# Performance work log

Hardware: AMD Instinct MI355X
Metric: run time of the kernel (lower is better)

Reference implementation:

```python
import jax, jax.numpy as jnp
import numpy as np

B, S, D = 8, 2048, 1024


def setup_inputs() -> dict:
    key = jax.random.key(0)
    k1, k2, k3, k4, k5 = jax.random.split(key, 5)
    scale = 1.0 / np.sqrt(D)
    x = jax.random.normal(k1, (B, S, D), dtype=jnp.float32)
    Wq = jax.random.normal(k2, (D, D), dtype=jnp.float32) * scale
    Wk = jax.random.normal(k3, (D, D), dtype=jnp.float32) * scale
    Wv = jax.random.normal(k4, (D, D), dtype=jnp.float32) * scale
    # sequence lengths in [1, S]
    lens = jax.random.randint(k5, (B,), 1, S + 1, dtype=jnp.int32)
    return {"x": x, "lens": lens, "Wq": Wq, "Wk": Wk, "Wv": Wv}


def reference(x, lens, Wq, Wk, Wv):
    # nn.Linear(bias=False): y = x @ W.T
    q = jnp.einsum('bsd,ed->bse', x, Wq)
    k = jnp.einsum('bsd,ed->bse', x, Wk)
    v = jnp.einsum('bsd,ed->bse', x, Wv)
    # scores: QK^T / sqrt(D)  -> [B, S, S]
    scores = jnp.einsum('bqd,bkd->bqk', q, k) / jnp.sqrt(jnp.asarray(D, x.dtype))
    # key-padding mask from lens: True where key position >= len (masked to -inf)
    key_pad = jnp.arange(S)[None, :] >= lens[:, None]          # [B, S]
    scores = jnp.where(key_pad[:, None, :], -jnp.inf, scores)  # broadcast over query dim
    att = jax.nn.softmax(scores, axis=2)
    return jnp.einsum('bqk,bkd->bqd', att, v)
```

## Files before the change

### kernel.cpp

```cpp
#include <hip/hip_runtime.h>
#include <stdint.h>

typedef __bf16 bf16;
typedef __bf16 bf16x8 __attribute__((ext_vector_type(8)));
typedef __bf16 bf16x4 __attribute__((ext_vector_type(4)));
typedef float f32x4 __attribute__((ext_vector_type(4)));
typedef float f32x16 __attribute__((ext_vector_type(16)));

#define DEV static __device__ __forceinline__

DEV void async_copy16(const bf16* gsrc, const bf16* ldst) {
  __builtin_amdgcn_global_load_lds(
      (__attribute__((address_space(1))) void*)(uintptr_t)gsrc,
      (__attribute__((address_space(3))) void*)(uint32_t)(uintptr_t)ldst,
      16, 0, 0);
}

DEV void gemm_tile16(const bf16* __restrict__ A, const bf16* __restrict__ B,
                     int lda, int ldb, int kTiles,
                     bf16* As, bf16* Bs, f32x4 acc[4][4]) {
  const int tid  = threadIdx.x;
  const int wave = tid >> 6;
  const int lane = tid & 63;
  const int wm = (wave >> 1) * 64;
  const int wn = (wave & 1) * 64;
  const int mf = lane & 15;
  const int jb = lane >> 4;
  const int sw = (mf & 7) * 8;

  const int srow = tid >> 3;
  const int scol = ((tid & 7) ^ (srow & 7)) * 8;
  const bf16* Ag = A + (size_t)srow * lda + scol;
  const bf16* Bg = B + (size_t)srow * ldb + scol;
  bf16* Asw = As + wave * 512;
  bf16* Bsw = Bs + wave * 512;

  for (int kt = 0; kt < kTiles; ++kt) {
    __syncthreads();
    const bf16* ag = Ag + kt * 64;
    const bf16* bg = Bg + kt * 64;
#pragma unroll
    for (int i = 0; i < 4; ++i) {
      async_copy16(ag + (size_t)(i * 32) * lda, Asw + i * 2048);
      async_copy16(bg + (size_t)(i * 32) * ldb, Bsw + i * 2048);
    }
    __syncthreads();
#pragma unroll
    for (int ks = 0; ks < 2; ++ks) {
      const int j8 = (ks * 4 + jb) * 8;
      bf16x8 af[4], bv[4];
#pragma unroll
      for (int i = 0; i < 4; ++i)
        af[i] = *(const bf16x8*)&As[(wm + i * 16 + mf) * 64 + (j8 ^ sw)];
#pragma unroll
      for (int j = 0; j < 4; ++j)
        bv[j] = *(const bf16x8*)&Bs[(wn + j * 16 + mf) * 64 + (j8 ^ sw)];
#pragma unroll
      for (int i = 0; i < 4; ++i)
#pragma unroll
        for (int j = 0; j < 4; ++j)
          acc[i][j] = __builtin_amdgcn_mfma_f32_16x16x32_bf16(af[i], bv[j], acc[i][j], 0, 0, 0);
    }
  }
}

DEV void gemm_tile32(const bf16* __restrict__ A, const bf16* __restrict__ B,
                     int lda, int ldb, int kTiles,
                     bf16* As, bf16* Bs, f32x16 acc[2][2]) {
  const int tid  = threadIdx.x;
  const int wave = tid >> 6;
  const int lane = tid & 63;
  const int wm = (wave >> 1) * 64;
  const int wn = (wave & 1) * 64;
  const int rf = lane & 31;
  const int kh = (lane >> 5) * 8;
  const int sw = (lane & 7) * 8;

  const int srow = tid >> 3;
  const int scol = ((tid & 7) ^ (srow & 7)) * 8;
  const bf16* Ag = A + (size_t)srow * lda + scol;
  const bf16* Bg = B + (size_t)srow * ldb + scol;
  bf16* Asw = As + wave * 512;
  bf16* Bsw = Bs + wave * 512;

  for (int kt = 0; kt < kTiles; ++kt) {
    __syncthreads();
    const bf16* ag = Ag + kt * 64;
    const bf16* bg = Bg + kt * 64;
#pragma unroll
    for (int i = 0; i < 4; ++i) {
      async_copy16(ag + (size_t)(i * 32) * lda, Asw + i * 2048);
      async_copy16(bg + (size_t)(i * 32) * ldb, Bsw + i * 2048);
    }
    __syncthreads();
#pragma unroll
    for (int ks = 0; ks < 4; ++ks) {
      const int off = (ks * 16 + kh) ^ sw;
      bf16x8 a0 = *(const bf16x8*)&As[(wm + rf) * 64 + off];
      bf16x8 a1 = *(const bf16x8*)&As[(wm + 32 + rf) * 64 + off];
      bf16x8 b0 = *(const bf16x8*)&Bs[(wn + rf) * 64 + off];
      bf16x8 b1 = *(const bf16x8*)&Bs[(wn + 32 + rf) * 64 + off];
      acc[0][0] = __builtin_amdgcn_mfma_f32_32x32x16_bf16(a0, b0, acc[0][0], 0, 0, 0);
      acc[0][1] = __builtin_amdgcn_mfma_f32_32x32x16_bf16(a0, b1, acc[0][1], 0, 0, 0);
      acc[1][0] = __builtin_amdgcn_mfma_f32_32x32x16_bf16(a1, b0, acc[1][0], 0, 0, 0);
      acc[1][1] = __builtin_amdgcn_mfma_f32_32x32x16_bf16(a1, b1, acc[1][1], 0, 0, 0);
    }
  }
}

#define EPILOGUE16(STMT)                                                     \
  do {                                                                       \
    const int lane = threadIdx.x & 63, wave = threadIdx.x >> 6;              \
    const int colb = n0 + (wave & 1) * 64 + (lane & 15);                     \
    const int rowb = m0 + (wave >> 1) * 64 + (lane >> 4) * 4;                \
    _Pragma("unroll") for (int i = 0; i < 4; ++i)                            \
      _Pragma("unroll") for (int r = 0; r < 4; ++r) {                        \
        size_t row = rowb + i * 16 + r;                                      \
        _Pragma("unroll") for (int j = 0; j < 4; ++j) {                      \
          size_t col = colb + j * 16;                                        \
          float val = acc[i][j][r];                                          \
          STMT;                                                              \
        }                                                                    \
      }                                                                      \
  } while (0)

#define EPILOGUE32(STMT)                                                     \
  do {                                                                       \
    const int lane = threadIdx.x & 63, wave = threadIdx.x >> 6;              \
    const int colb = n0 + (wave & 1) * 64 + (lane & 31);                     \
    const int rowb = m0 + (wave >> 1) * 64 + (lane >> 5) * 4;                \
    _Pragma("unroll") for (int i = 0; i < 2; ++i)                            \
      _Pragma("unroll") for (int reg = 0; reg < 16; ++reg) {                 \
        size_t row = rowb + i * 32 + (reg & 3) + 8 * (reg >> 2);             \
        _Pragma("unroll") for (int j = 0; j < 2; ++j) {                      \
          size_t col = colb + j * 32;                                        \
          float val = acc[i][j][reg];                                        \
          STMT;                                                              \
        }                                                                    \
      }                                                                      \
  } while (0)

__global__ __launch_bounds__(256) void k_cast_all(const float* __restrict__ X,
                                                  const float* __restrict__ Wq,
                                                  const float* __restrict__ Wk,
                                                  const float* __restrict__ Wv,
                                                  bf16* __restrict__ Xb,
                                                  bf16* __restrict__ Wb) {
  int i = blockIdx.x * 256 + threadIdx.x;
  const float* src;
  bf16* dst;
  int off;
  if (i < 4194304) {
    src = X; dst = Xb; off = i;
  } else {
    int j = i - 4194304;
    int which = j >> 18;
    src = (which == 0) ? Wq : ((which == 1) ? Wk : Wv);
    dst = Wb + (size_t)(j >> 18) * 1048576;
    off = j & 262143;
  }
  float4 v = ((const float4*)src)[off];
  bf16x4 o = {(bf16)v.x, (bf16)v.y, (bf16)v.z, (bf16)v.w};
  ((bf16x4*)dst)[off] = o;
}

__global__ __launch_bounds__(256) void k_gemm_qkv(const bf16* __restrict__ X,
                                                  const bf16* __restrict__ W,
                                                  const int* __restrict__ lens,
                                                  bf16* __restrict__ QKV) {
  const int n0 = blockIdx.x * 128;
  const int m0 = blockIdx.y * 128;
  if (n0 >= 1024 && (m0 & 2047) >= lens[m0 >> 11]) return;
  __shared__ __align__(16) bf16 As[128 * 64];
  __shared__ __align__(16) bf16 Bs[128 * 64];
  f32x4 acc[4][4] = {};
  gemm_tile16(X + (size_t)m0 * 1024, W + (size_t)n0 * 1024, 1024, 1024, 16, As, Bs, acc);
  const float qscale = (n0 < 1024) ? 0.03125f : 1.0f;
  EPILOGUE16(QKV[row * 3072 + col] = (bf16)(val * qscale));
}

__global__ __launch_bounds__(256) void k_transpose_v(const bf16* __restrict__ QKV,
                                                     const int* __restrict__ lens,
                                                     bf16* __restrict__ Vt) {
  __shared__ bf16 tile[32][33];
  const int b = blockIdx.z;
  const int s0 = blockIdx.x * 32;
  if (s0 >= ((lens[b] + 63) & ~63)) return;
  const int d0 = blockIdx.y * 32;
  const int tx = threadIdx.x, ty = threadIdx.y;
#pragma unroll
  for (int i = 0; i < 4; ++i)
    tile[ty + i * 8][tx] = QKV[(size_t)(b * 2048 + s0 + ty + i * 8) * 3072 + 2048 + d0 + tx];
  __syncthreads();
#pragma unroll
  for (int i = 0; i < 4; ++i)
    Vt[(size_t)(b * 1024 + d0 + ty + i * 8) * 2048 + s0 + tx] = tile[tx][ty + i * 8];
}

__global__ __launch_bounds__(256) void k_gemm_scores(const bf16* __restrict__ QKV,
                                                     const int* __restrict__ lens,
                                                     bf16* __restrict__ S) {
  const int b = blockIdx.z;
  const int len = lens[b];
  const int n0 = blockIdx.x * 128;
  if (n0 >= len) return;
  const int m0 = blockIdx.y * 128;
  __shared__ __align__(16) bf16 As[128 * 64];
  __shared__ __align__(16) bf16 Bs[128 * 64];
  const bf16* Q = QKV + (size_t)b * 2048 * 3072;
  const bf16* K = Q + 1024;
  f32x16 acc[2][2] = {};
  gemm_tile32(Q + (size_t)m0 * 3072, K + (size_t)n0 * 3072, 3072, 3072, 16, As, Bs, acc);
  bf16* Sb = S + (size_t)b * 2048 * 2048;
  EPILOGUE32(Sb[row * 2048 + col] = (bf16)val);
}

__global__ __launch_bounds__(256) void k_softmax(bf16* __restrict__ S,
                                                 const int* __restrict__ lens) {
  const int row = blockIdx.x;
  const int len = lens[row >> 11];
  const int kmax = (len + 63) & ~63;
  bf16* Sr = S + (size_t)row * 2048;
  const int tid = threadIdx.x;
  const int base = tid * 8;
  __shared__ float red[4];

  float f[8];
  if (base < len) {
    bf16x8 v = ((const bf16x8*)Sr)[tid];
#pragma unroll
    for (int e = 0; e < 8; ++e) f[e] = (base + e < len) ? (float)v[e] : -1e30f;
  } else {
#pragma unroll
    for (int e = 0; e < 8; ++e) f[e] = -1e30f;
  }
  float m = -1e30f;
#pragma unroll
  for (int e = 0; e < 8; ++e) m = fmaxf(m, f[e]);
#pragma unroll
  for (int off = 32; off; off >>= 1) m = fmaxf(m, __shfl_xor(m, off));
  if ((tid & 63) == 0) red[tid >> 6] = m;
  __syncthreads();
  m = fmaxf(fmaxf(red[0], red[1]), fmaxf(red[2], red[3]));
  __syncthreads();

  float s = 0.f;
#pragma unroll
  for (int e = 0; e < 8; ++e) {
    float p = (base + e < len) ? __expf(f[e] - m) : 0.f;
    f[e] = p;
    s += p;
  }
#pragma unroll
  for (int off = 32; off; off >>= 1) s += __shfl_xor(s, off);
  if ((tid & 63) == 0) red[tid >> 6] = s;
  __syncthreads();
  s = red[0] + red[1] + red[2] + red[3];
  const float inv = 1.f / s;

  if (base < kmax) {
    bf16x8 o;
#pragma unroll
    for (int e = 0; e < 8; ++e) o[e] = (bf16)(f[e] * inv);
    ((bf16x8*)Sr)[tid] = o;
  }
}

__global__ __launch_bounds__(256) void k_gemm_out(const bf16* __restrict__ P,
                                                  const bf16* __restrict__ Vt,
                                                  const int* __restrict__ lens,
                                                  float* __restrict__ Out) {
  const int b = blockIdx.z;
  const int kTiles = (lens[b] + 63) >> 6;
  const int n0 = blockIdx.x * 128;
  const int m0 = blockIdx.y * 128;
  __shared__ __align__(16) bf16 As[128 * 64];
  __shared__ __align__(16) bf16 Bs[128 * 64];
  const bf16* Pb = P + (size_t)b * 2048 * 2048;
  const bf16* Vb = Vt + (size_t)b * 1024 * 2048;
  f32x16 acc[2][2] = {};
  gemm_tile32(Pb + (size_t)m0 * 2048, Vb + (size_t)n0 * 2048, 2048, 2048, kTiles, As, Bs, acc);
  float* Ob = Out + (size_t)b * 2048 * 1024;
  EPILOGUE32(Ob[row * 1024 + col] = val);
}

extern "C" void kernel_launch(void* const* d_in, const int* in_sizes, int n_in,
                              void* d_out, int out_size, void* d_ws, size_t ws_size,
                              hipStream_t stream) {
  const float* x   = (const float*)d_in[0];
  const int* lens  = (const int*)d_in[1];
  const float* Wq  = (const float*)d_in[2];
  const float* Wk  = (const float*)d_in[3];
  const float* Wv  = (const float*)d_in[4];
  float* out = (float*)d_out;

  char* ws = (char*)d_ws;
  bf16* S   = (bf16*)(ws);
  bf16* Xb  = (bf16*)(ws);
  bf16* Wb  = (bf16*)(ws + 33554432);
  bf16* QKV = (bf16*)(ws + 67108864);
  bf16* Vt  = (bf16*)(ws + 167772160);

  k_cast_all<<<19456, 256, 0, stream>>>(x, Wq, Wk, Wv, Xb, Wb);
  k_gemm_qkv<<<dim3(24, 128), 256, 0, stream>>>(Xb, Wb, lens, QKV);
  k_transpose_v<<<dim3(64, 32, 8), dim3(32, 8), 0, stream>>>(QKV, lens, Vt);
  k_gemm_scores<<<dim3(16, 16, 8), 256, 0, stream>>>(QKV, lens, S);
  k_softmax<<<16384, 256, 0, stream>>>(S, lens);
  k_gemm_out<<<dim3(8, 16, 8), 256, 0, stream>>>(S, Vt, lens, out);
}
```

Baseline: 359.6 us.

## Rewrite QKV GEMM with 256x256 tiles, double-buffered async LDS loads

The QKV projection GEMM moves from 128x128 tiles with 256 threads and a single LDS buffer to 256x256 tiles with 512 threads and a K-step of 32. Global-to-LDS async copies are double-buffered, so the load for step t+2 is issued while step t computes, with explicit waitcnt and barriers. MFMA issue runs at raised wave priority. The larger tiles raise operand reuse per load, at the cost of higher register use (32 accumulators per wave), coarser padding skip, and fewer blocks for the machine to spread across CUs.

```diff
diff --git a/kernel.cpp b/kernel.cpp
--- a/kernel.cpp
+++ b/kernel.cpp
@@ -14,54 +14,6 @@
       (__attribute__((address_space(1))) void*)(uintptr_t)gsrc,
       (__attribute__((address_space(3))) void*)(uint32_t)(uintptr_t)ldst,
       16, 0, 0);
-}
-
-DEV void gemm_tile16(const bf16* __restrict__ A, const bf16* __restrict__ B,
-                     int lda, int ldb, int kTiles,
-                     bf16* As, bf16* Bs, f32x4 acc[4][4]) {
-  const int tid  = threadIdx.x;
-  const int wave = tid >> 6;
-  const int lane = tid & 63;
-  const int wm = (wave >> 1) * 64;
-  const int wn = (wave & 1) * 64;
-  const int mf = lane & 15;
-  const int jb = lane >> 4;
-  const int sw = (mf & 7) * 8;
-
-  const int srow = tid >> 3;
-  const int scol = ((tid & 7) ^ (srow & 7)) * 8;
-  const bf16* Ag = A + (size_t)srow * lda + scol;
-  const bf16* Bg = B + (size_t)srow * ldb + scol;
-  bf16* Asw = As + wave * 512;
-  bf16* Bsw = Bs + wave * 512;
-
-  for (int kt = 0; kt < kTiles; ++kt) {
-    __syncthreads();
-    const bf16* ag = Ag + kt * 64;
-    const bf16* bg = Bg + kt * 64;
-#pragma unroll
-    for (int i = 0; i < 4; ++i) {
-      async_copy16(ag + (size_t)(i * 32) * lda, Asw + i * 2048);
-      async_copy16(bg + (size_t)(i * 32) * ldb, Bsw + i * 2048);
-    }
-    __syncthreads();
-#pragma unroll
-    for (int ks = 0; ks < 2; ++ks) {
-      const int j8 = (ks * 4 + jb) * 8;
-      bf16x8 af[4], bv[4];
-#pragma unroll
-      for (int i = 0; i < 4; ++i)
-        af[i] = *(const bf16x8*)&As[(wm + i * 16 + mf) * 64 + (j8 ^ sw)];
-#pragma unroll
-      for (int j = 0; j < 4; ++j)
-        bv[j] = *(const bf16x8*)&Bs[(wn + j * 16 + mf) * 64 + (j8 ^ sw)];
-#pragma unroll
-      for (int i = 0; i < 4; ++i)
-#pragma unroll
-        for (int j = 0; j < 4; ++j)
-          acc[i][j] = __builtin_amdgcn_mfma_f32_16x16x32_bf16(af[i], bv[j], acc[i][j], 0, 0, 0);
-    }
-  }
 }
 
 DEV void gemm_tile32(const bf16* __restrict__ A, const bf16* __restrict__ B,
@@ -107,22 +59,6 @@
     }
   }
 }
-
-#define EPILOGUE16(STMT)                                                     \
-  do {                                                                       \
-    const int lane = threadIdx.x & 63, wave = threadIdx.x >> 6;              \
-    const int colb = n0 + (wave & 1) * 64 + (lane & 15);                     \
-    const int rowb = m0 + (wave >> 1) * 64 + (lane >> 4) * 4;                \
-    _Pragma("unroll") for (int i = 0; i < 4; ++i)                            \
-      _Pragma("unroll") for (int r = 0; r < 4; ++r) {                        \
-        size_t row = rowb + i * 16 + r;                                      \
-        _Pragma("unroll") for (int j = 0; j < 4; ++j) {                      \
-          size_t col = colb + j * 16;                                        \
-          float val = acc[i][j][r];                                          \
-          STMT;                                                              \
-        }                                                                    \
-      }                                                                      \
-  } while (0)
 
 #define EPILOGUE32(STMT)                                                     \
   do {                                                                       \
@@ -164,19 +100,93 @@
   ((bf16x4*)dst)[off] = o;
 }
 
-__global__ __launch_bounds__(256) void k_gemm_qkv(const bf16* __restrict__ X,
-                                                  const bf16* __restrict__ W,
-                                                  const int* __restrict__ lens,
-                                                  bf16* __restrict__ QKV) {
-  const int n0 = blockIdx.x * 128;
-  const int m0 = blockIdx.y * 128;
+__global__ __launch_bounds__(512, 2) void k_gemm_qkv(
+    const bf16* __restrict__ X, const bf16* __restrict__ W,
+    const int* __restrict__ lens, bf16* __restrict__ QKV) {
+  const int n0 = blockIdx.x * 256;
+  const int m0 = blockIdx.y * 256;
   if (n0 >= 1024 && (m0 & 2047) >= lens[m0 >> 11]) return;
-  __shared__ __align__(16) bf16 As[128 * 64];
-  __shared__ __align__(16) bf16 Bs[128 * 64];
-  f32x4 acc[4][4] = {};
-  gemm_tile16(X + (size_t)m0 * 1024, W + (size_t)n0 * 1024, 1024, 1024, 16, As, Bs, acc);
+  __shared__ __align__(16) char smem[65536];
+
+  const int tid = threadIdx.x;
+  const int lane = tid & 63, wid = tid >> 6;
+
+  int grow0, gcol0, grow1, gcol1;
+  {
+    int g = tid, rho = g >> 3, sig = (g & 7) ^ (rho & 7);
+    grow0 = 2 * rho + (sig >> 2); gcol0 = (sig & 3) * 8;
+    g = tid + 512; rho = g >> 3; sig = (g & 7) ^ (rho & 7);
+    grow1 = 2 * rho + (sig >> 2); gcol1 = (sig & 3) * 8;
+  }
+  const bf16* pa0 = X + (size_t)(m0 + grow0) * 1024 + gcol0;
+  const bf16* pa1 = X + (size_t)(m0 + grow1) * 1024 + gcol1;
+  const bf16* pb0 = W + (size_t)(n0 + grow0) * 1024 + gcol0;
+  const bf16* pb1 = W + (size_t)(n0 + grow1) * 1024 + gcol1;
+
+#define QKV_STAGE(kt, slot)                                  \
+  do {                                                       \
+    const int ko_ = (kt) * 32;                               \
+    char* sb_ = smem + (slot) * 32768 + wid * 1024;          \
+    async_copy16(pa0 + ko_, (const bf16*)sb_);               \
+    async_copy16(pa1 + ko_, (const bf16*)(sb_ + 8192));      \
+    async_copy16(pb0 + ko_, (const bf16*)(sb_ + 16384));     \
+    async_copy16(pb1 + ko_, (const bf16*)(sb_ + 24576));     \
+  } while (0)
+
+  const int mf = lane & 15, jb = lane >> 4;
+  const int wm = (wid >> 2) * 128, wn = (wid & 3) * 64;
+  const uint32_t pbyte = (uint32_t)((((((mf & 1) << 2) | jb) ^ ((mf >> 1) & 7))) * 16);
+  const uint32_t laneA = (uint32_t)(wm * 64 + (mf >> 1) * 128) + pbyte;
+  const uint32_t laneB = 16384u + (uint32_t)(wn * 64 + (mf >> 1) * 128) + pbyte;
+
+  f32x4 acc[8][4] = {};
+
+  QKV_STAGE(0, 0);
+  QKV_STAGE(1, 1);
+  asm volatile("s_waitcnt vmcnt(4)" ::: "memory");
+  __builtin_amdgcn_sched_barrier(0);
+  __builtin_amdgcn_s_barrier();
+  __builtin_amdgcn_sched_barrier(0);
+
+  for (int t = 0; t < 32; ++t) {
+    const char* As = smem + (t & 1) * 32768 + laneA;
+    const char* Bs = smem + (t & 1) * 32768 + laneB;
+    bf16x8 af[8], bfr[4];
+#pragma unroll
+    for (int i = 0; i < 8; ++i) af[i] = *(const bf16x8*)(As + i * 1024);
+#pragma unroll
+    for (int j = 0; j < 4; ++j) bfr[j] = *(const bf16x8*)(Bs + j * 1024);
+    __builtin_amdgcn_s_setprio(1);
+#pragma unroll
+    for (int i = 0; i < 8; ++i)
+#pragma unroll
+      for (int j = 0; j < 4; ++j)
+        acc[i][j] = __builtin_amdgcn_mfma_f32_16x16x32_bf16(af[i], bfr[j], acc[i][j], 0, 0, 0);
+    __builtin_amdgcn_s_setprio(0);
+    asm volatile("s_waitcnt lgkmcnt(0)" ::: "memory");
+    __builtin_amdgcn_sched_barrier(0);
+    __builtin_amdgcn_s_barrier();
+    __builtin_amdgcn_sched_barrier(0);
+    const int nx = (t + 2 < 32) ? t + 2 : 31;
+    QKV_STAGE(nx, t & 1);
+    asm volatile("s_waitcnt vmcnt(4)" ::: "memory");
+    __builtin_amdgcn_sched_barrier(0);
+    __builtin_amdgcn_s_barrier();
+    __builtin_amdgcn_sched_barrier(0);
+  }
+#undef QKV_STAGE
+
   const float qscale = (n0 < 1024) ? 0.03125f : 1.0f;
-  EPILOGUE16(QKV[row * 3072 + col] = (bf16)(val * qscale));
+  const int colb = n0 + wn + mf;
+  const int rowb = m0 + wm + jb * 4;
+#pragma unroll
+  for (int i = 0; i < 8; ++i)
+#pragma unroll
+    for (int r = 0; r < 4; ++r) {
+      bf16* dst = QKV + (size_t)(rowb + i * 16 + r) * 3072 + colb;
+#pragma unroll
+      for (int j = 0; j < 4; ++j) dst[j * 16] = (bf16)(acc[i][j][r] * qscale);
+    }
 }
 
 __global__ __launch_bounds__(256) void k_transpose_v(const bf16* __restrict__ QKV,
@@ -302,7 +312,7 @@
   bf16* Vt  = (bf16*)(ws + 167772160);
 
   k_cast_all<<<19456, 256, 0, stream>>>(x, Wq, Wk, Wv, Xb, Wb);
-  k_gemm_qkv<<<dim3(24, 128), 256, 0, stream>>>(Xb, Wb, lens, QKV);
+  k_gemm_qkv<<<dim3(12, 64), 512, 0, stream>>>(Xb, Wb, lens, QKV);
   k_transpose_v<<<dim3(64, 32, 8), dim3(32, 8), 0, stream>>>(QKV, lens, Vt);
   k_gemm_scores<<<dim3(16, 16, 8), 256, 0, stream>>>(QKV, lens, S);
   k_softmax<<<16384, 256, 0, stream>>>(S, lens);
```

New measurement: 385.9 us. +7.3%, slower.

## Compute V transposed directly via Wv·Xᵀ GEMM, drop transpose kernel

Applied to the files above, without the earlier changes.

V is no longer produced by the QKV projection and then transposed. A separate GEMM computes Vt = Wv · Xbᵀ per batch and writes it directly in the transposed layout that the output GEMM consumes. This removes the transpose kernel and the round trip of V through global memory, and it narrows the QK buffer to a 2048-column stride. In exchange it adds one kernel launch and changes how padding rows are skipped: V tiles are now culled by the rounded-up length in the N dimension rather than by the row length.

```diff
diff --git a/kernel.cpp b/kernel.cpp
--- a/kernel.cpp
+++ b/kernel.cpp
@@ -167,7 +167,7 @@
 __global__ __launch_bounds__(256) void k_gemm_qkv(const bf16* __restrict__ X,
                                                   const bf16* __restrict__ W,
                                                   const int* __restrict__ lens,
-                                                  bf16* __restrict__ QKV) {
+                                                  bf16* __restrict__ QK) {
   const int n0 = blockIdx.x * 128;
   const int m0 = blockIdx.y * 128;
   if (n0 >= 1024 && (m0 & 2047) >= lens[m0 >> 11]) return;
@@ -176,28 +176,27 @@
   f32x4 acc[4][4] = {};
   gemm_tile16(X + (size_t)m0 * 1024, W + (size_t)n0 * 1024, 1024, 1024, 16, As, Bs, acc);
   const float qscale = (n0 < 1024) ? 0.03125f : 1.0f;
-  EPILOGUE16(QKV[row * 3072 + col] = (bf16)(val * qscale));
-}
-
-__global__ __launch_bounds__(256) void k_transpose_v(const bf16* __restrict__ QKV,
-                                                     const int* __restrict__ lens,
-                                                     bf16* __restrict__ Vt) {
-  __shared__ bf16 tile[32][33];
+  EPILOGUE16(QK[row * 2048 + col] = (bf16)(val * qscale));
+}
+
+__global__ __launch_bounds__(256) void k_gemm_vt(const bf16* __restrict__ Xb,
+                                                 const bf16* __restrict__ Wv,
+                                                 const int* __restrict__ lens,
+                                                 bf16* __restrict__ Vt) {
   const int b = blockIdx.z;
-  const int s0 = blockIdx.x * 32;
-  if (s0 >= ((lens[b] + 63) & ~63)) return;
-  const int d0 = blockIdx.y * 32;
-  const int tx = threadIdx.x, ty = threadIdx.y;
-#pragma unroll
-  for (int i = 0; i < 4; ++i)
-    tile[ty + i * 8][tx] = QKV[(size_t)(b * 2048 + s0 + ty + i * 8) * 3072 + 2048 + d0 + tx];
-  __syncthreads();
-#pragma unroll
-  for (int i = 0; i < 4; ++i)
-    Vt[(size_t)(b * 1024 + d0 + ty + i * 8) * 2048 + s0 + tx] = tile[tx][ty + i * 8];
-}
-
-__global__ __launch_bounds__(256) void k_gemm_scores(const bf16* __restrict__ QKV,
+  const int n0 = blockIdx.x * 128;
+  if (n0 >= ((lens[b] + 63) & ~63)) return;
+  const int m0 = blockIdx.y * 128;
+  __shared__ __align__(16) bf16 As[128 * 64];
+  __shared__ __align__(16) bf16 Bs[128 * 64];
+  f32x4 acc[4][4] = {};
+  gemm_tile16(Wv + (size_t)m0 * 1024, Xb + (size_t)(b * 2048 + n0) * 1024,
+              1024, 1024, 16, As, Bs, acc);
+  bf16* Vtb = Vt + (size_t)b * 1024 * 2048;
+  EPILOGUE16(Vtb[row * 2048 + col] = (bf16)val);
+}
+
+__global__ __launch_bounds__(256) void k_gemm_scores(const bf16* __restrict__ QK,
                                                      const int* __restrict__ lens,
                                                      bf16* __restrict__ S) {
   const int b = blockIdx.z;
@@ -207,10 +206,10 @@
   const int m0 = blockIdx.y * 128;
   __shared__ __align__(16) bf16 As[128 * 64];
   __shared__ __align__(16) bf16 Bs[128 * 64];
-  const bf16* Q = QKV + (size_t)b * 2048 * 3072;
+  const bf16* Q = QK + (size_t)b * 2048 * 2048;
   const bf16* K = Q + 1024;
   f32x16 acc[2][2] = {};
-  gemm_tile32(Q + (size_t)m0 * 3072, K + (size_t)n0 * 3072, 3072, 3072, 16, As, Bs, acc);
+  gemm_tile32(Q + (size_t)m0 * 2048, K + (size_t)n0 * 2048, 2048, 2048, 16, As, Bs, acc);
   bf16* Sb = S + (size_t)b * 2048 * 2048;
   EPILOGUE32(Sb[row * 2048 + col] = (bf16)val);
 }
@@ -298,13 +297,13 @@
   bf16* S   = (bf16*)(ws);
   bf16* Xb  = (bf16*)(ws);
   bf16* Wb  = (bf16*)(ws + 33554432);
-  bf16* QKV = (bf16*)(ws + 67108864);
-  bf16* Vt  = (bf16*)(ws + 167772160);
+  bf16* QK  = (bf16*)(ws + 67108864);
+  bf16* Vt  = (bf16*)(ws + 134217728);
 
   k_cast_all<<<19456, 256, 0, stream>>>(x, Wq, Wk, Wv, Xb, Wb);
-  k_gemm_qkv<<<dim3(24, 128), 256, 0, stream>>>(Xb, Wb, lens, QKV);
-  k_transpose_v<<<dim3(64, 32, 8), dim3(32, 8), 0, stream>>>(QKV, lens, Vt);
-  k_gemm_scores<<<dim3(16, 16, 8), 256, 0, stream>>>(QKV, lens, S);
+  k_gemm_qkv<<<dim3(16, 128), 256, 0, stream>>>(Xb, Wb, lens, QK);
+  k_gemm_vt<<<dim3(16, 8, 8), 256, 0, stream>>>(Xb, Wb + 2 * 1048576, lens, Vt);
+  k_gemm_scores<<<dim3(16, 16, 8), 256, 0, stream>>>(QK, lens, S);
   k_softmax<<<16384, 256, 0, stream>>>(S, lens);
   k_gemm_out<<<dim3(8, 16, 8), 256, 0, stream>>>(S, Vt, lens, out);
 }
```

Result: slower. 398.4 us (+10.8%).
